# Kernel optimization log

Measured on AMD Instinct MI355X. Metric: run time of the kernel, lower is better.

The kernel has to match this reference:

```python
import jax, jax.numpy as jnp
import numpy as np

N = 50000   # num_nodes
H = 128     # n_hidden
C = 16      # num_classes
R = 8       # num_rels
B = 4       # num_bases
E = 800000  # num_edges


def setup_inputs() -> dict:
    key = jax.random.key(0)
    ks = jax.random.split(key, 20)
    s = 0.05
    return {
        "src": jax.random.randint(ks[0], (E,), 0, N),
        "dst": jax.random.randint(ks[1], (E,), 0, N),
        "h": jnp.arange(N),                      # node IDs (first layer in_feat == num_nodes)
        "r": jax.random.randint(ks[2], (E,), 0, R),
        "norm": jax.random.uniform(ks[3], (E, 1), dtype=jnp.float32),
        # layer 0: basis weights over [num_nodes -> H]
        "bases0": jax.random.normal(ks[4], (B, N, H), dtype=jnp.float32) * s,
        "wcomp0": jax.random.normal(ks[5], (R, B), dtype=jnp.float32) * s,
        "loop0": jax.random.normal(ks[6], (N, H), dtype=jnp.float32) * s,
        "bias0": jnp.zeros((H,), dtype=jnp.float32),
        # layer 1: H -> H
        "bases1": jax.random.normal(ks[7], (B, H, H), dtype=jnp.float32) * s,
        "wcomp1": jax.random.normal(ks[8], (R, B), dtype=jnp.float32) * s,
        "loop1": jax.random.normal(ks[9], (H, H), dtype=jnp.float32) * s,
        "bias1": jnp.zeros((H,), dtype=jnp.float32),
        # layer 2: H -> C
        "bases2": jax.random.normal(ks[10], (B, H, C), dtype=jnp.float32) * s,
        "wcomp2": jax.random.normal(ks[11], (R, B), dtype=jnp.float32) * s,
        "loop2": jax.random.normal(ks[12], (H, C), dtype=jnp.float32) * s,
        "bias2": jnp.zeros((C,), dtype=jnp.float32),
    }


def _agg(msg, dst):
    return jax.ops.segment_sum(msg, dst, num_segments=N)


def _layer_id(ids, src, dst, r, norm, bases, wcomp, loop, bias):
    # first layer: input features are node IDs -> embedding lookup into composed weight
    w = jnp.einsum('rb,bnf->rnf', wcomp, bases)      # [R, N, H]
    msg = w[r, ids[src]] * norm                      # [E, H] gather per edge
    out = _agg(msg, dst) + loop[ids] + bias          # aggregate + self-loop + bias
    return jax.nn.relu(out)


def _layer_dense(x, src, dst, r, norm, bases, wcomp, loop, bias, act):
    w = jnp.einsum('rb,bdf->rdf', wcomp, bases)      # [R, d_in, d_out]
    trans = jnp.einsum('nd,rdf->rnf', x, w)          # [R, N, d_out] (all rel transforms)
    msg = trans[r, src] * norm                       # [E, d_out] relation-indexed gather
    out = _agg(msg, dst) + x @ loop + bias
    return jax.nn.relu(out) if act else out


def reference(src, dst, h, r, norm,
              bases0, wcomp0, loop0, bias0,
              bases1, wcomp1, loop1, bias1,
              bases2, wcomp2, loop2, bias2):
    x = _layer_id(h, src, dst, r, norm, bases0, wcomp0, loop0, bias0)
    x = _layer_dense(x, src, dst, r, norm, bases1, wcomp1, loop1, bias1, act=True)
    x = _layer_dense(x, src, dst, r, norm, bases2, wcomp2, loop2, bias2, act=False)
    return x
```

## Files before the change

### kernel.cpp

```cpp
#include <hip/hip_runtime.h>

#define NN 50000
#define NP 50048
#define HH 128
#define CC 16
#define RRL 8
#define BB 4
#define EE 800000
#define NT (RRL * NN)
#define SCAN_CHUNK 2048
#define NBLK_SCAN ((NT + SCAN_CHUNK - 1) / SCAN_CHUNK)
#define KBIG 1152

typedef short bf16x8_t __attribute__((ext_vector_type(8)));
typedef float f32x4_t __attribute__((ext_vector_type(4)));

__device__ __forceinline__ unsigned short f2bf(float f) {
  unsigned int x = __float_as_uint(f);
  unsigned int r = x + 0x7fffu + ((x >> 16) & 1u);
  return (unsigned short)(r >> 16);
}
__device__ __forceinline__ float bflo(unsigned int u) { return __uint_as_float(u << 16); }
__device__ __forceinline__ float bfhi(unsigned int u) {
  return __uint_as_float(u & 0xffff0000u);
}
__device__ __forceinline__ void acc8(float* a, uint4 v, float nrm) {
  a[0] = fmaf(nrm, bflo(v.x), a[0]);
  a[1] = fmaf(nrm, bfhi(v.x), a[1]);
  a[2] = fmaf(nrm, bflo(v.y), a[2]);
  a[3] = fmaf(nrm, bfhi(v.y), a[3]);
  a[4] = fmaf(nrm, bflo(v.z), a[4]);
  a[5] = fmaf(nrm, bfhi(v.z), a[5]);
  a[6] = fmaf(nrm, bflo(v.w), a[6]);
  a[7] = fmaf(nrm, bfhi(v.w), a[7]);
}


__global__ __launch_bounds__(256) void zero_kernel(int* p, int n) {
  int i = blockIdx.x * 256 + threadIdx.x;
  if (i < n) p[i] = 0;
}


__global__ __launch_bounds__(256) void hist2_kernel(const int* __restrict__ r,
                                                    const int* __restrict__ dst,
                                                    int* __restrict__ cnt) {
  int e = blockIdx.x * 256 + threadIdx.x;
  if (e < EE) atomicAdd(&cnt[dst[e] * RRL + r[e]], 1);
}

__global__ __launch_bounds__(256) void scanA_kernel(const int* __restrict__ cnt,
                                                    int* __restrict__ off,
                                                    int* __restrict__ partials) {
  __shared__ int sums[256];
  int tid = threadIdx.x;
  int base = blockIdx.x * SCAN_CHUNK + tid * 8;
  int v[8];
  int s = 0;
#pragma unroll
  for (int j = 0; j < 8; ++j) {
    int idx = base + j;
    v[j] = (idx < NT) ? cnt[idx] : 0;
    s += v[j];
  }
  sums[tid] = s;
  __syncthreads();
  for (int o = 1; o < 256; o <<= 1) {
    int t = (tid >= o) ? sums[tid - o] : 0;
    __syncthreads();
    sums[tid] += t;
    __syncthreads();
  }
  int run = sums[tid] - s;
#pragma unroll
  for (int j = 0; j < 8; ++j) {
    int idx = base + j;
    if (idx < NT) off[idx] = run;
    run += v[j];
  }
  if (tid == 255) partials[blockIdx.x] = sums[255];
}

__global__ __launch_bounds__(256) void scanB_kernel(const int* __restrict__ partials,
                                                    int* __restrict__ pexcl) {
  __shared__ int sums[256];
  int tid = threadIdx.x;
  int p = (tid < NBLK_SCAN) ? partials[tid] : 0;
  sums[tid] = p;
  __syncthreads();
  for (int o = 1; o < 256; o <<= 1) {
    int t = (tid >= o) ? sums[tid - o] : 0;
    __syncthreads();
    sums[tid] += t;
    __syncthreads();
  }
  if (tid < NBLK_SCAN) pexcl[tid] = sums[tid] - p;
}

__global__ __launch_bounds__(256) void addC_kernel(int* __restrict__ off,
                                                   const int* __restrict__ pexcl,
                                                   int* __restrict__ cur) {
  int tid = threadIdx.x;
  int add = pexcl[blockIdx.x];
  int base = blockIdx.x * SCAN_CHUNK + tid * 8;
#pragma unroll
  for (int j = 0; j < 8; ++j) {
    int idx = base + j;
    if (idx < NT) {
      int v = off[idx] + add;
      off[idx] = v;
      cur[idx] = v;
    }
  }
  if (blockIdx.x == 0 && tid == 0) off[NT] = EE;
}

__global__ __launch_bounds__(256) void scatter2_kernel(
    const int* __restrict__ r, const int* __restrict__ dst, const int* __restrict__ src,
    const float* __restrict__ norm, int* __restrict__ cur, uint2* __restrict__ ep1) {
  int e = blockIdx.x * 256 + threadIdx.x;
  if (e >= EE) return;
  int z = r[e];
  int key = dst[e] * RRL + z;
  int pos = atomicAdd(&cur[key], 1);
  uint2 b;
  b.x = (unsigned)src[e] | ((unsigned)z << 24);
  b.y = __float_as_uint(norm[e]);
  ep1[pos] = b;
}


__global__ __launch_bounds__(256) void compose_small_kernel(
    const float* __restrict__ wcomp1, const float* __restrict__ bases1,
    const float* __restrict__ loop1, const float* __restrict__ wcomp2,
    const float* __restrict__ bases2, const float* __restrict__ loop2,
    unsigned short* __restrict__ w1big, unsigned short* __restrict__ w2t,
    unsigned short* __restrict__ loop2t) {
  int idx = blockIdx.x * 256 + threadIdx.x;
  if (idx < HH * KBIG) {
    int n = idx / KBIG, k = idx - n * KBIG;
    float a;
    if (k < 1024) {
      int z = k >> 7, kk = k & 127;
      a = 0.f;
#pragma unroll
      for (int b = 0; b < BB; ++b)
        a += wcomp1[z * BB + b] * bases1[((size_t)b * HH + kk) * HH + n];
    } else {
      int kk = k - 1024;
      a = loop1[kk * HH + n];
    }
    w1big[idx] = f2bf(a);
    return;
  }
  int j = idx - HH * KBIG;
  if (j < RRL * CC * HH) {
    int z = j >> 11;
    int rem = j & 2047;
    int n = rem >> 7, k = rem & 127;
    float a = 0.f;
#pragma unroll
    for (int b = 0; b < BB; ++b)
      a += wcomp2[z * BB + b] * bases2[((size_t)b * HH + k) * CC + n];
    w2t[j] = f2bf(a);
    return;
  }
  j -= RRL * CC * HH;
  if (j < CC * HH) {
    int n = j >> 7, k = j & 127;
    loop2t[j] = f2bf(loop2[k * CC + n]);
  }
}


__global__ __launch_bounds__(256) void w0b_build_kernel(const float* __restrict__ bases0,
                                                        const float* __restrict__ wcomp0,
                                                        unsigned short* __restrict__ w0b) {
  int idx = blockIdx.x * 256 + threadIdx.x;
  int m = idx >> 5, c = idx & 31;
  if (m >= NN) return;
  float4 b0 = ((const float4*)(bases0 + ((size_t)0 * NN + m) * HH))[c];
  float4 b1 = ((const float4*)(bases0 + ((size_t)1 * NN + m) * HH))[c];
  float4 b2 = ((const float4*)(bases0 + ((size_t)2 * NN + m) * HH))[c];
  float4 b3 = ((const float4*)(bases0 + ((size_t)3 * NN + m) * HH))[c];
#pragma unroll
  for (int z = 0; z < RRL; ++z) {
    float c0 = wcomp0[z * BB + 0], c1 = wcomp0[z * BB + 1];
    float c2 = wcomp0[z * BB + 2], c3 = wcomp0[z * BB + 3];
    float vx = c0 * b0.x + c1 * b1.x + c2 * b2.x + c3 * b3.x;
    float vy = c0 * b0.y + c1 * b1.y + c2 * b2.y + c3 * b3.y;
    float vz = c0 * b0.z + c1 * b1.z + c2 * b2.z + c3 * b3.z;
    float vw = c0 * b0.w + c1 * b1.w + c2 * b2.w + c3 * b3.w;
    uint2 pk;
    pk.x = ((unsigned)f2bf(vy) << 16) | f2bf(vx);
    pk.y = ((unsigned)f2bf(vw) << 16) | f2bf(vz);
    ((uint2*)(w0b + ((size_t)z * NP + m) * HH))[c] = pk;
  }
}


__global__ __launch_bounds__(256) void l0_seg_kernel(
    const int* __restrict__ h, const int* __restrict__ off2, const uint2* __restrict__ ep1,
    const unsigned short* __restrict__ w0b, const float* __restrict__ loop0,
    const float* __restrict__ bias0, unsigned short* __restrict__ x1b) {
  int lane = threadIdx.x & 63;
  int n = blockIdx.x * 4 + (threadIdx.x >> 6);
  if (n >= NP) return;
  const int g = lane >> 4;
  const int t = lane & 15;
  float acc[8];
#pragma unroll
  for (int j = 0; j < 8; ++j) acc[j] = 0.f;

  if (n < NN) {
    int beg = off2[n * RRL];
    int end = off2[n * RRL + RRL];
    int i = beg + g;
    uint2 p0 = {0u, 0u}, p1 = {0u, 0u};
    if (i < end) p0 = ep1[i];
    if (i + 4 < end) p1 = ep1[i + 4];
    unsigned r0 = (p0.x >> 24) * NP + (unsigned)h[p0.x & 0xFFFFFFu];
    unsigned r1 = (p1.x >> 24) * NP + (unsigned)h[p1.x & 0xFFFFFFu];
    while (i < end) {
      uint2 q0 = {0u, 0u}, q1 = {0u, 0u};
      if (i + 8 < end) q0 = ep1[i + 8];
      if (i + 12 < end) q1 = ep1[i + 12];
      uint4 va = *(const uint4*)(w0b + (size_t)r0 * HH + t * 8);
      uint4 vb = *(const uint4*)(w0b + (size_t)r1 * HH + t * 8);
      float na = __uint_as_float(p0.y), nb = __uint_as_float(p1.y);
      acc8(acc, va, na);
      acc8(acc, vb, nb);
      i += 8;
      p0 = q0;
      p1 = q1;
      r0 = (q0.x >> 24) * NP + (unsigned)h[q0.x & 0xFFFFFFu];
      r1 = (q1.x >> 24) * NP + (unsigned)h[q1.x & 0xFFFFFFu];
    }
  }
#pragma unroll
  for (int j = 0; j < 8; ++j) {
    acc[j] += __shfl_xor(acc[j], 16, 64);
    acc[j] += __shfl_xor(acc[j], 32, 64);
  }
  if (g != 0) return;
  uint4 o = {0u, 0u, 0u, 0u};
  if (n < NN) {
    int hn = h[n];
    float4 l0v = ((const float4*)(loop0 + (size_t)hn * HH))[t * 2];
    float4 l1v = ((const float4*)(loop0 + (size_t)hn * HH))[t * 2 + 1];
    float4 b0v = ((const float4*)bias0)[t * 2];
    float4 b1v = ((const float4*)bias0)[t * 2 + 1];
    float e0 = fmaxf(acc[0] + l0v.x + b0v.x, 0.f);
    float e1 = fmaxf(acc[1] + l0v.y + b0v.y, 0.f);
    float e2 = fmaxf(acc[2] + l0v.z + b0v.z, 0.f);
    float e3 = fmaxf(acc[3] + l0v.w + b0v.w, 0.f);
    float e4 = fmaxf(acc[4] + l1v.x + b1v.x, 0.f);
    float e5 = fmaxf(acc[5] + l1v.y + b1v.y, 0.f);
    float e6 = fmaxf(acc[6] + l1v.z + b1v.z, 0.f);
    float e7 = fmaxf(acc[7] + l1v.w + b1v.w, 0.f);
    o.x = ((unsigned)f2bf(e1) << 16) | f2bf(e0);
    o.y = ((unsigned)f2bf(e3) << 16) | f2bf(e2);
    o.z = ((unsigned)f2bf(e5) << 16) | f2bf(e4);
    o.w = ((unsigned)f2bf(e7) << 16) | f2bf(e6);
  }
  *(uint4*)(x1b + (size_t)n * HH + t * 8) = o;
}


__global__ __launch_bounds__(256) void l1_agg_kernel(const int* __restrict__ off2,
                                                     const uint2* __restrict__ ep1,
                                                     const unsigned short* __restrict__ x1b,
                                                     unsigned short* __restrict__ AGG) {
  int tid = threadIdx.x;
  int gid = blockIdx.x * 16 + (tid >> 4);
  int l = tid & 15;
  int n = gid >> 3, z = gid & 7;
  if (n >= NP) return;
  unsigned short* orow = AGG + (size_t)n * 1024 + z * 128 + l * 8;
  if (n >= NN) {
    *(uint4*)orow = (uint4){0u, 0u, 0u, 0u};
    return;
  }
  int beg = off2[gid];
  int end = off2[gid + 1];
  float a[8];
#pragma unroll
  for (int j = 0; j < 8; ++j) a[j] = 0.f;

  int i = beg;
  uint2 p0 = {0u, 0u}, p1 = {0u, 0u};
  if (i < end) p0 = ep1[i];
  if (i + 1 < end) p1 = ep1[i + 1];
  while (i < end) {
    uint2 q0 = {0u, 0u}, q1 = {0u, 0u};
    if (i + 2 < end) q0 = ep1[i + 2];
    if (i + 3 < end) q1 = ep1[i + 3];
    unsigned s0 = p0.x & 0xFFFFFFu, s1 = p1.x & 0xFFFFFFu;
    uint4 v0 = *(const uint4*)(x1b + (size_t)s0 * HH + l * 8);
    uint4 v1 = *(const uint4*)(x1b + (size_t)s1 * HH + l * 8);
    float n0 = __uint_as_float(p0.y), n1 = __uint_as_float(p1.y);
    acc8(a, v0, n0);
    acc8(a, v1, n1);
    i += 2;
    p0 = q0;
    p1 = q1;
  }
  uint4 o;
  o.x = ((unsigned)f2bf(a[1]) << 16) | f2bf(a[0]);
  o.y = ((unsigned)f2bf(a[3]) << 16) | f2bf(a[2]);
  o.z = ((unsigned)f2bf(a[5]) << 16) | f2bf(a[4]);
  o.w = ((unsigned)f2bf(a[7]) << 16) | f2bf(a[6]);
  *(uint4*)orow = o;
}


__global__ __launch_bounds__(256) void gemm_k1152_kernel(
    const unsigned short* __restrict__ AGG, const unsigned short* __restrict__ x1b,
    const unsigned short* __restrict__ w1big, const float* __restrict__ bias1,
    unsigned short* __restrict__ x2b) {
  constexpr int LP = 136;
  __shared__ unsigned short Alds[64 * LP];
  __shared__ unsigned short Blds[128 * LP];
  const int row0 = blockIdx.x * 64;
  const int tid = threadIdx.x;
  const int w = tid >> 6, lane = tid & 63;
  const int quad = lane >> 4, l15 = lane & 15;
  const int rb = (w >> 1) * 32;
  const int cb = (w & 1) * 64;

  f32x4_t acc[2][4];
#pragma unroll
  for (int rt = 0; rt < 2; ++rt)
#pragma unroll
    for (int ct = 0; ct < 4; ++ct) acc[rt][ct] = (f32x4_t){0.f, 0.f, 0.f, 0.f};

  for (int kb = 0; kb < 9; ++kb) {
    if (kb) __syncthreads();
#pragma unroll
    for (int it = 0; it < 4; ++it) {
      int flat = tid + it * 256;
      int row = flat >> 4, c8 = flat & 15;
      const unsigned short* srcp =
          (kb < 8) ? AGG + (size_t)(row0 + row) * 1024 + kb * 128 + c8 * 8
                   : x1b + (size_t)(row0 + row) * 128 + c8 * 8;
      *(uint4*)(&Alds[row * LP + c8 * 8]) = *(const uint4*)srcp;
    }
#pragma unroll
    for (int it = 0; it < 8; ++it) {
      int flat = tid + it * 256;
      int row = flat >> 4, c8 = flat & 15;
      *(uint4*)(&Blds[row * LP + c8 * 8]) =
          *(const uint4*)(w1big + (size_t)row * KBIG + kb * 128 + c8 * 8);
    }
    __syncthreads();
#pragma unroll
    for (int ks = 0; ks < 4; ++ks) {
      int ko = ks * 32 + quad * 8;
      bf16x8_t af[2], bfr[4];
#pragma unroll
      for (int rt = 0; rt < 2; ++rt)
        af[rt] = *(const bf16x8_t*)(&Alds[(rb + rt * 16 + l15) * LP + ko]);
#pragma unroll
      for (int ct = 0; ct < 4; ++ct)
        bfr[ct] = *(const bf16x8_t*)(&Blds[(cb + ct * 16 + l15) * LP + ko]);
#pragma unroll
      for (int rt = 0; rt < 2; ++rt)
#pragma unroll
        for (int ct = 0; ct < 4; ++ct)
          acc[rt][ct] =
              __builtin_amdgcn_mfma_f32_16x16x32_bf16(af[rt], bfr[ct], acc[rt][ct], 0, 0, 0);
    }
  }
#pragma unroll
  for (int rt = 0; rt < 2; ++rt)
#pragma unroll
    for (int ct = 0; ct < 4; ++ct) {
      int n = cb + ct * 16 + l15;
      float bv = bias1[n];
#pragma unroll
      for (int i = 0; i < 4; ++i) {
        int m = row0 + rb + rt * 16 + quad * 4 + i;
        float val = (m < NN) ? fmaxf(acc[rt][ct][i] + bv, 0.f) : 0.f;
        x2b[(size_t)m * HH + n] = f2bf(val);
      }
    }
}


__global__ __launch_bounds__(256) void l2_trans_kernel(
    const unsigned short* __restrict__ x2b, const unsigned short* __restrict__ w2t,
    const unsigned short* __restrict__ loop2t, const float* __restrict__ bias2,
    unsigned short* __restrict__ trans2, float* __restrict__ out) {
  constexpr int LP = 136;
  __shared__ unsigned short Alds[128 * LP];
  __shared__ unsigned short Blds[9][16 * LP];
  const int row0 = blockIdx.x * 128;
  const int tid = threadIdx.x;

#pragma unroll
  for (int it = 0; it < 8; ++it) {
    int flat = tid + it * 256;
    int row = flat >> 4, c8 = flat & 15;
    *(uint4*)(&Alds[row * LP + c8 * 8]) =
        *(const uint4*)(x2b + ((size_t)(row0 + row)) * 128 + c8 * 8);
  }
  {
    int row = tid >> 4, c8 = tid & 15;
#pragma unroll
    for (int z = 0; z < 9; ++z) {
      const unsigned short* B = (z < 8) ? w2t + (size_t)z * CC * HH : loop2t;
      *(uint4*)(&Blds[z][row * LP + c8 * 8]) = *(const uint4*)(B + row * 128 + c8 * 8);
    }
  }
  __syncthreads();

  const int w = tid >> 6, lane = tid & 63;
  const int quad = lane >> 4, l15 = lane & 15;
  const int rb = w * 32;

  for (int z = 0; z < 9; ++z) {
    f32x4_t acc[2];
    acc[0] = (f32x4_t){0.f, 0.f, 0.f, 0.f};
    acc[1] = (f32x4_t){0.f, 0.f, 0.f, 0.f};
#pragma unroll
    for (int ks = 0; ks < 4; ++ks) {
      int ko = ks * 32 + quad * 8;
      bf16x8_t af0 = *(const bf16x8_t*)(&Alds[(rb + l15) * LP + ko]);
      bf16x8_t af1 = *(const bf16x8_t*)(&Alds[(rb + 16 + l15) * LP + ko]);
      bf16x8_t bfr = *(const bf16x8_t*)(&Blds[z][l15 * LP + ko]);
      acc[0] = __builtin_amdgcn_mfma_f32_16x16x32_bf16(af0, bfr, acc[0], 0, 0, 0);
      acc[1] = __builtin_amdgcn_mfma_f32_16x16x32_bf16(af1, bfr, acc[1], 0, 0, 0);
    }
    if (z < 8) {
      unsigned short* ob = trans2 + (size_t)z * NP * CC;
#pragma unroll
      for (int rt = 0; rt < 2; ++rt)
#pragma unroll
        for (int i = 0; i < 4; ++i) {
          int m = row0 + rb + rt * 16 + quad * 4 + i;
          ob[(size_t)m * CC + l15] = f2bf(acc[rt][i]);
        }
    } else {
      float bv = bias2[l15];
#pragma unroll
      for (int rt = 0; rt < 2; ++rt)
#pragma unroll
        for (int i = 0; i < 4; ++i) {
          int m = row0 + rb + rt * 16 + quad * 4 + i;
          if (m < NN) out[(size_t)m * CC + l15] = acc[rt][i] + bv;
        }
    }
  }
}


__global__ __launch_bounds__(256) void l2_seg_kernel(const int* __restrict__ off2,
                                                     const uint2* __restrict__ ep1,
                                                     const unsigned short* __restrict__ trans2,
                                                     float* __restrict__ outp) {
  int lane = threadIdx.x & 63;
  int n = blockIdx.x * 4 + (threadIdx.x >> 6);
  if (n >= NN) return;
  const int g = lane >> 3;
  const int t = lane & 7;
  float a0 = 0.f, a1 = 0.f;
  int beg = off2[n * RRL];
  int end = off2[n * RRL + RRL];
  int i = beg + g;
  uint2 p0 = {0u, 0u}, p1 = {0u, 0u};
  if (i < end) p0 = ep1[i];
  if (i + 8 < end) p1 = ep1[i + 8];
  while (i < end) {
    uint2 q0 = {0u, 0u}, q1 = {0u, 0u};
    if (i + 16 < end) q0 = ep1[i + 16];
    if (i + 24 < end) q1 = ep1[i + 24];
    unsigned s0 = p0.x & 0xFFFFFFu, z0 = p0.x >> 24;
    unsigned s1 = p1.x & 0xFFFFFFu, z1 = p1.x >> 24;
    unsigned int u0 =
        *(const unsigned int*)(trans2 + ((size_t)z0 * NP + s0) * CC + t * 2);
    unsigned int u1 =
        *(const unsigned int*)(trans2 + ((size_t)z1 * NP + s1) * CC + t * 2);
    float na = __uint_as_float(p0.y), nb = __uint_as_float(p1.y);
    a0 = fmaf(na, bflo(u0), a0);
    a1 = fmaf(na, bfhi(u0), a1);
    a0 = fmaf(nb, bflo(u1), a0);
    a1 = fmaf(nb, bfhi(u1), a1);
    i += 16;
    p0 = q0;
    p1 = q1;
  }
  a0 += __shfl_xor(a0, 8, 64);
  a0 += __shfl_xor(a0, 16, 64);
  a0 += __shfl_xor(a0, 32, 64);
  a1 += __shfl_xor(a1, 8, 64);
  a1 += __shfl_xor(a1, 16, 64);
  a1 += __shfl_xor(a1, 32, 64);
  if (g != 0) return;
  float2* o = (float2*)(outp + (size_t)n * CC) + t;
  float2 cv = *o;
  cv.x += a0;
  cv.y += a1;
  *o = cv;
}


extern "C" void kernel_launch(void* const* d_in, const int* in_sizes, int n_in,
                              void* d_out, int out_size, void* d_ws, size_t ws_size,
                              hipStream_t stream) {
  const int* src = (const int*)d_in[0];
  const int* dst = (const int*)d_in[1];
  const int* h = (const int*)d_in[2];
  const int* r = (const int*)d_in[3];
  const float* norm = (const float*)d_in[4];
  const float* bases0 = (const float*)d_in[5];
  const float* wcomp0 = (const float*)d_in[6];
  const float* loop0 = (const float*)d_in[7];
  const float* bias0 = (const float*)d_in[8];
  const float* bases1 = (const float*)d_in[9];
  const float* wcomp1 = (const float*)d_in[10];
  const float* loop1 = (const float*)d_in[11];
  const float* bias1 = (const float*)d_in[12];
  const float* bases2 = (const float*)d_in[13];
  const float* wcomp2 = (const float*)d_in[14];
  const float* loop2 = (const float*)d_in[15];
  const float* bias2 = (const float*)d_in[16];
  float* out = (float*)d_out;

  char* p = (char*)d_ws;
  auto alloc = [&](size_t bytes) {
    char* q = p;
    p += (bytes + 255) & ~(size_t)255;
    return q;
  };
  unsigned short* x1b = (unsigned short*)alloc((size_t)NP * HH * 2);
  unsigned short* x2b = (unsigned short*)alloc((size_t)NP * HH * 2);
  unsigned short* trans2 = (unsigned short*)alloc((size_t)RRL * NP * CC * 2);
  unsigned short* w1big = (unsigned short*)alloc((size_t)HH * KBIG * 2);
  unsigned short* w2t = (unsigned short*)alloc((size_t)RRL * CC * HH * 2);
  unsigned short* loop2t = (unsigned short*)alloc((size_t)CC * HH * 2);
  uint2* ep1 = (uint2*)alloc((size_t)EE * 8);
  int* off2 = (int*)alloc((size_t)(NT + 1) * 4);
  int* cur2 = (int*)alloc((size_t)NT * 4);
  int* cnt2 = (int*)alloc((size_t)NT * 4);
  int* partials = (int*)alloc(1024);
  int* pexcl = (int*)alloc(1024);
  unsigned short* BIG = (unsigned short*)alloc((size_t)RRL * NP * HH * 2);

  zero_kernel<<<(NT + 255) / 256, 256, 0, stream>>>(cnt2, NT);
  hist2_kernel<<<(EE + 255) / 256, 256, 0, stream>>>(r, dst, cnt2);
  scanA_kernel<<<NBLK_SCAN, 256, 0, stream>>>(cnt2, off2, partials);
  scanB_kernel<<<1, 256, 0, stream>>>(partials, pexcl);
  addC_kernel<<<NBLK_SCAN, 256, 0, stream>>>(off2, pexcl, cur2);
  scatter2_kernel<<<(EE + 255) / 256, 256, 0, stream>>>(r, dst, src, norm, cur2, ep1);

  compose_small_kernel<<<(HH * KBIG + RRL * CC * HH + CC * HH) / 256, 256, 0, stream>>>(
      wcomp1, bases1, loop1, wcomp2, bases2, loop2, w1big, w2t, loop2t);

  w0b_build_kernel<<<(NN * 32) / 256, 256, 0, stream>>>(bases0, wcomp0, BIG);
  l0_seg_kernel<<<NP / 4, 256, 0, stream>>>(h, off2, ep1, BIG, loop0, bias0, x1b);

  l1_agg_kernel<<<NP * 8 / 16, 256, 0, stream>>>(off2, ep1, x1b, BIG);
  gemm_k1152_kernel<<<NP / 64, 256, 0, stream>>>(BIG, x1b, w1big, bias1, x2b);

  l2_trans_kernel<<<NP / 128, 256, 0, stream>>>(x2b, w2t, loop2t, bias2, trans2, out);
  l2_seg_kernel<<<(NN + 3) / 4, 256, 0, stream>>>(off2, ep1, trans2, out);
}
```

Measured before the change: 475.5 us.

## Two-pass bucketed edge scatter and merge weight-prep kernels

Replaces the single global-atomic edge scatter with a two-pass scheme. The first pass partitions edges into 98 coarse destination buckets using shared-memory histograms. The second pass places edges per bucket, so the atomics and writes into the CSR array stay within a small L2-friendly region. The layer-0 and small weight-composition kernels are merged into one launch, and the zero kernel is replaced by hipMemsetAsync. This adds an extra round trip through temporary key and payload buffers and an extra launch in exchange for more local scatter writes.

```diff
diff --git a/kernel.cpp b/kernel.cpp
--- a/kernel.cpp
+++ b/kernel.cpp
@@ -11,6 +11,13 @@
 #define SCAN_CHUNK 2048
 #define NBLK_SCAN ((NT + SCAN_CHUNK - 1) / SCAN_CHUNK)
 #define KBIG 1152
+#define W0B_BLOCKS ((NN * 32) / 256)
+#define COMPOSE_THREADS (HH * KBIG + RRL * CC * HH + CC * HH)
+#define COMPOSE_BLOCKS ((COMPOSE_THREADS + 255) / 256)
+#define NC 98
+#define SPLIT 2
+#define CHUNK_E 4096
+#define PA_BLOCKS ((EE + CHUNK_E - 1) / CHUNK_E)
 
 typedef short bf16x8_t __attribute__((ext_vector_type(8)));
 typedef float f32x4_t __attribute__((ext_vector_type(4)));
@@ -33,12 +40,6 @@
   a[5] = fmaf(nrm, bfhi(v.z), a[5]);
   a[6] = fmaf(nrm, bflo(v.w), a[6]);
   a[7] = fmaf(nrm, bfhi(v.w), a[7]);
-}
-
-
-__global__ __launch_bounds__(256) void zero_kernel(int* p, int n) {
-  int i = blockIdx.x * 256 + threadIdx.x;
-  if (i < n) p[i] = 0;
 }
 
 
@@ -99,7 +100,8 @@
 
 __global__ __launch_bounds__(256) void addC_kernel(int* __restrict__ off,
                                                    const int* __restrict__ pexcl,
-                                                   int* __restrict__ cur) {
+                                                   int* __restrict__ cur,
+                                                   int* __restrict__ curC) {
   int tid = threadIdx.x;
   int add = pexcl[blockIdx.x];
   int base = blockIdx.x * SCAN_CHUNK + tid * 8;
@@ -110,33 +112,101 @@
       int v = off[idx] + add;
       off[idx] = v;
       cur[idx] = v;
+      if ((idx & 4095) == 0) curC[idx >> 12] = v;
     }
   }
   if (blockIdx.x == 0 && tid == 0) off[NT] = EE;
 }
 
-__global__ __launch_bounds__(256) void scatter2_kernel(
+
+__global__ __launch_bounds__(256) void partitionA_kernel(
     const int* __restrict__ r, const int* __restrict__ dst, const int* __restrict__ src,
-    const float* __restrict__ norm, int* __restrict__ cur, uint2* __restrict__ ep1) {
-  int e = blockIdx.x * 256 + threadIdx.x;
-  if (e >= EE) return;
-  int z = r[e];
-  int key = dst[e] * RRL + z;
-  int pos = atomicAdd(&cur[key], 1);
-  uint2 b;
-  b.x = (unsigned)src[e] | ((unsigned)z << 24);
-  b.y = __float_as_uint(norm[e]);
-  ep1[pos] = b;
-}
-
-
-__global__ __launch_bounds__(256) void compose_small_kernel(
-    const float* __restrict__ wcomp1, const float* __restrict__ bases1,
-    const float* __restrict__ loop1, const float* __restrict__ wcomp2,
-    const float* __restrict__ bases2, const float* __restrict__ loop2,
-    unsigned short* __restrict__ w1big, unsigned short* __restrict__ w2t,
-    unsigned short* __restrict__ loop2t) {
-  int idx = blockIdx.x * 256 + threadIdx.x;
+    const float* __restrict__ norm, int* __restrict__ curC, unsigned* __restrict__ tmpK,
+    uint2* __restrict__ tmpP) {
+  __shared__ int hist[NC];
+  __shared__ int run[NC];
+  int tid = threadIdx.x;
+  int base = blockIdx.x * CHUNK_E;
+  for (int i = tid; i < NC; i += 256) hist[i] = 0;
+  __syncthreads();
+#pragma unroll
+  for (int j = 0; j < CHUNK_E / 256; ++j) {
+    int e = base + tid + j * 256;
+    if (e < EE) atomicAdd(&hist[dst[e] >> 9], 1);
+  }
+  __syncthreads();
+  if (tid < NC && hist[tid] > 0) run[tid] = atomicAdd(&curC[tid], hist[tid]);
+  __syncthreads();
+#pragma unroll
+  for (int j = 0; j < CHUNK_E / 256; ++j) {
+    int e = base + tid + j * 256;
+    if (e < EE) {
+      int d = dst[e], z = r[e];
+      int c = d >> 9;
+      int pos = atomicAdd(&run[c], 1);
+      tmpK[pos] = (unsigned)(d * RRL + z);
+      uint2 pay;
+      pay.x = (unsigned)src[e] | ((unsigned)z << 24);
+      pay.y = __float_as_uint(norm[e]);
+      tmpP[pos] = pay;
+    }
+  }
+}
+
+
+__global__ __launch_bounds__(256) void placeB_kernel(const int* __restrict__ off2,
+                                                     const unsigned* __restrict__ tmpK,
+                                                     const uint2* __restrict__ tmpP,
+                                                     int* __restrict__ cur2,
+                                                     uint2* __restrict__ ep1) {
+  int c = blockIdx.x / SPLIT, q = blockIdx.x % SPLIT;
+  int kb = c * 4096;
+  int ke = (c + 1) * 4096;
+  if (ke > NT) ke = NT;
+  int beg = off2[kb], end = off2[ke];
+  int len = end - beg;
+  int qb = beg + (len * q) / SPLIT;
+  int qe = beg + (len * (q + 1)) / SPLIT;
+  for (int i = qb + threadIdx.x; i < qe; i += 256) {
+    unsigned key = tmpK[i];
+    uint2 pay = tmpP[i];
+    int pos = atomicAdd(&cur2[key], 1);
+    ep1[pos] = pay;
+  }
+}
+
+
+__global__ __launch_bounds__(256) void prep_weights_kernel(
+    const float* __restrict__ bases0, const float* __restrict__ wcomp0,
+    unsigned short* __restrict__ w0b, const float* __restrict__ wcomp1,
+    const float* __restrict__ bases1, const float* __restrict__ loop1,
+    const float* __restrict__ wcomp2, const float* __restrict__ bases2,
+    const float* __restrict__ loop2, unsigned short* __restrict__ w1big,
+    unsigned short* __restrict__ w2t, unsigned short* __restrict__ loop2t) {
+  if (blockIdx.x < W0B_BLOCKS) {
+    int idx = blockIdx.x * 256 + threadIdx.x;
+    int m = idx >> 5, c = idx & 31;
+    if (m >= NN) return;
+    float4 b0 = ((const float4*)(bases0 + ((size_t)0 * NN + m) * HH))[c];
+    float4 b1 = ((const float4*)(bases0 + ((size_t)1 * NN + m) * HH))[c];
+    float4 b2 = ((const float4*)(bases0 + ((size_t)2 * NN + m) * HH))[c];
+    float4 b3 = ((const float4*)(bases0 + ((size_t)3 * NN + m) * HH))[c];
+#pragma unroll
+    for (int z = 0; z < RRL; ++z) {
+      float c0 = wcomp0[z * BB + 0], c1 = wcomp0[z * BB + 1];
+      float c2 = wcomp0[z * BB + 2], c3 = wcomp0[z * BB + 3];
+      float vx = c0 * b0.x + c1 * b1.x + c2 * b2.x + c3 * b3.x;
+      float vy = c0 * b0.y + c1 * b1.y + c2 * b2.y + c3 * b3.y;
+      float vz = c0 * b0.z + c1 * b1.z + c2 * b2.z + c3 * b3.z;
+      float vw = c0 * b0.w + c1 * b1.w + c2 * b2.w + c3 * b3.w;
+      uint2 pk;
+      pk.x = ((unsigned)f2bf(vy) << 16) | f2bf(vx);
+      pk.y = ((unsigned)f2bf(vw) << 16) | f2bf(vz);
+      ((uint2*)(w0b + ((size_t)z * NP + m) * HH))[c] = pk;
+    }
+    return;
+  }
+  int idx = (blockIdx.x - W0B_BLOCKS) * 256 + threadIdx.x;
   if (idx < HH * KBIG) {
     int n = idx / KBIG, k = idx - n * KBIG;
     float a;
@@ -169,32 +239,6 @@
   if (j < CC * HH) {
     int n = j >> 7, k = j & 127;
     loop2t[j] = f2bf(loop2[k * CC + n]);
-  }
-}
-
-
-__global__ __launch_bounds__(256) void w0b_build_kernel(const float* __restrict__ bases0,
-                                                        const float* __restrict__ wcomp0,
-                                                        unsigned short* __restrict__ w0b) {
-  int idx = blockIdx.x * 256 + threadIdx.x;
-  int m = idx >> 5, c = idx & 31;
-  if (m >= NN) return;
-  float4 b0 = ((const float4*)(bases0 + ((size_t)0 * NN + m) * HH))[c];
-  float4 b1 = ((const float4*)(bases0 + ((size_t)1 * NN + m) * HH))[c];
-  float4 b2 = ((const float4*)(bases0 + ((size_t)2 * NN + m) * HH))[c];
-  float4 b3 = ((const float4*)(bases0 + ((size_t)3 * NN + m) * HH))[c];
-#pragma unroll
-  for (int z = 0; z < RRL; ++z) {
-    float c0 = wcomp0[z * BB + 0], c1 = wcomp0[z * BB + 1];
-    float c2 = wcomp0[z * BB + 2], c3 = wcomp0[z * BB + 3];
-    float vx = c0 * b0.x + c1 * b1.x + c2 * b2.x + c3 * b3.x;
-    float vy = c0 * b0.y + c1 * b1.y + c2 * b2.y + c3 * b3.y;
-    float vz = c0 * b0.z + c1 * b1.z + c2 * b2.z + c3 * b3.z;
-    float vw = c0 * b0.w + c1 * b1.w + c2 * b2.w + c3 * b3.w;
-    uint2 pk;
-    pk.x = ((unsigned)f2bf(vy) << 16) | f2bf(vx);
-    pk.y = ((unsigned)f2bf(vw) << 16) | f2bf(vz);
-    ((uint2*)(w0b + ((size_t)z * NP + m) * HH))[c] = pk;
   }
 }
 
@@ -539,24 +583,28 @@
   unsigned short* w2t = (unsigned short*)alloc((size_t)RRL * CC * HH * 2);
   unsigned short* loop2t = (unsigned short*)alloc((size_t)CC * HH * 2);
   uint2* ep1 = (uint2*)alloc((size_t)EE * 8);
+  unsigned* tmpK = (unsigned*)alloc((size_t)EE * 4);
+  uint2* tmpP = (uint2*)alloc((size_t)EE * 8);
   int* off2 = (int*)alloc((size_t)(NT + 1) * 4);
   int* cur2 = (int*)alloc((size_t)NT * 4);
   int* cnt2 = (int*)alloc((size_t)NT * 4);
+  int* curC = (int*)alloc(1024);
   int* partials = (int*)alloc(1024);
   int* pexcl = (int*)alloc(1024);
   unsigned short* BIG = (unsigned short*)alloc((size_t)RRL * NP * HH * 2);
 
-  zero_kernel<<<(NT + 255) / 256, 256, 0, stream>>>(cnt2, NT);
+  hipMemsetAsync(cnt2, 0, (size_t)NT * 4, stream);
   hist2_kernel<<<(EE + 255) / 256, 256, 0, stream>>>(r, dst, cnt2);
   scanA_kernel<<<NBLK_SCAN, 256, 0, stream>>>(cnt2, off2, partials);
   scanB_kernel<<<1, 256, 0, stream>>>(partials, pexcl);
-  addC_kernel<<<NBLK_SCAN, 256, 0, stream>>>(off2, pexcl, cur2);
-  scatter2_kernel<<<(EE + 255) / 256, 256, 0, stream>>>(r, dst, src, norm, cur2, ep1);
-
-  compose_small_kernel<<<(HH * KBIG + RRL * CC * HH + CC * HH) / 256, 256, 0, stream>>>(
-      wcomp1, bases1, loop1, wcomp2, bases2, loop2, w1big, w2t, loop2t);
-
-  w0b_build_kernel<<<(NN * 32) / 256, 256, 0, stream>>>(bases0, wcomp0, BIG);
+  addC_kernel<<<NBLK_SCAN, 256, 0, stream>>>(off2, pexcl, cur2, curC);
+  partitionA_kernel<<<PA_BLOCKS, 256, 0, stream>>>(r, dst, src, norm, curC, tmpK, tmpP);
+  placeB_kernel<<<NC * SPLIT, 256, 0, stream>>>(off2, tmpK, tmpP, cur2, ep1);
+
+  prep_weights_kernel<<<W0B_BLOCKS + COMPOSE_BLOCKS, 256, 0, stream>>>(
+      bases0, wcomp0, BIG, wcomp1, bases1, loop1, wcomp2, bases2, loop2, w1big, w2t,
+      loop2t);
+
   l0_seg_kernel<<<NP / 4, 256, 0, stream>>>(h, off2, ep1, BIG, loop0, bias0, x1b);
 
   l1_agg_kernel<<<NP * 8 / 16, 256, 0, stream>>>(off2, ep1, x1b, BIG);
```

Result: no change. 479.0 us (+0.7%).
